# Kernel optimization log

Hardware: AMD Instinct MI355X
Metric: run time of the kernel (lower is better)

The kernel has to match this reference:

```python
import jax, jax.numpy as jnp
import numpy as np

N = 50000
E = 800000
H = 4
C = 64
IN = 61
NEG_SLOPE = 0.2


def setup_inputs() -> dict:
    key = jax.random.key(0)
    ks = jax.random.split(key, 20)
    x = jax.random.normal(ks[0], (N, IN), dtype=jnp.float32)
    edge_index = jax.random.randint(ks[1], (2, E), 0, N, dtype=jnp.int64)

    def glorot(k, shape):
        fan = shape[0] + shape[-1] if len(shape) == 2 else shape[-1] * 2
        s = jnp.sqrt(6.0 / fan)
        return jax.random.uniform(k, shape, jnp.float32, -s, s)

    dims = [IN, H * C, H * C]
    params = {}
    for i, din in enumerate(dims):
        params[f'w{i}'] = glorot(ks[2 + 4 * i], (din, H * C))
        params[f'att_src{i}'] = glorot(ks[3 + 4 * i], (H, C))
        params[f'att_dst{i}'] = glorot(ks[4 + 4 * i], (H, C))
        params[f'b{i}'] = jnp.zeros((H * C,), jnp.float32)
    params['head_w1'] = glorot(ks[14], (H * C, C))
    params['head_b1'] = jnp.zeros((C,), jnp.float32)
    params['head_w2'] = glorot(ks[15], (C, 1))
    params['head_b2'] = jnp.zeros((1,), jnp.float32)
    return dict(x=x, edge_index=edge_index, **params)


def _gat_layer(x, W, att_src, att_dst, bias, src, dst):
    # Linear transform -> [N, H, C]
    h = (x @ W).reshape(N, H, C)
    # Per-node attention logits
    a_src = jnp.einsum('nhc,hc->nh', h, att_src)  # [N, H]
    a_dst = jnp.einsum('nhc,hc->nh', h, att_dst)
    # Per-edge score, leaky relu
    e = jax.nn.leaky_relu(a_src[src] + a_dst[dst], NEG_SLOPE)  # [Etot, H]
    # Segment softmax over incoming edges of each dst node
    m = jax.ops.segment_max(e, dst, num_segments=N)  # [N, H]
    ex = jnp.exp(e - m[dst])
    denom = jax.ops.segment_sum(ex, dst, num_segments=N)
    alpha = ex / denom[dst]  # [Etot, H]
    # Scatter-aggregate messages
    out = jax.ops.segment_sum(h[src] * alpha[:, :, None], dst, num_segments=N)  # [N, H, C]
    return out.reshape(N, H * C) + bias


def reference(x, edge_index, w0, att_src0, att_dst0, b0,
              w1, att_src1, att_dst1, b1,
              w2, att_src2, att_dst2, b2,
              head_w1, head_b1, head_w2, head_b2):
    # PyG GATConv adds self-loops by default
    loop = jnp.arange(N, dtype=edge_index.dtype)
    src = jnp.concatenate([edge_index[0], loop])
    dst = jnp.concatenate([edge_index[1], loop])

    layers = [(w0, att_src0, att_dst0, b0),
              (w1, att_src1, att_dst1, b1),
              (w2, att_src2, att_dst2, b2)]
    h = x
    for (W, a_s, a_d, b) in layers:
        h = _gat_layer(h, W, a_s, a_d, b, src, dst)
        h = jax.nn.elu(h)  # dropout is identity in eval mode
    # MLP head
    h = jax.nn.relu(h @ head_w1 + head_b1)
    out = (h @ head_w2 + head_b2).squeeze(-1)  # [N]
    return out
```

## Files before the change

### kernel.cpp

```cpp
#include <hip/hip_runtime.h>
#include <cstdint>
#include <cstddef>

#define NN   50000
#define EE   800000
#define ETOT (EE + NN)
#define HC   256
#define NEG_SLOPE 0.2f
#define SENT_WORDS 25000
#define SENT_VAL 0x42C80000u

typedef __attribute__((ext_vector_type(8))) short g4_bf16x8;
typedef __attribute__((ext_vector_type(4))) float g4_f32x4;

__device__ __forceinline__ float g4_bf2f(unsigned short h) {
    union { unsigned int u; float f; } v;
    v.u = ((unsigned int)h) << 16;
    return v.f;
}
__device__ __forceinline__ unsigned short g4_f2bf(float f) {
    union { float f; unsigned int u; } v;
    v.f = f;
    unsigned int u = v.u;
    u += 0x7fffu + ((u >> 16) & 1u);
    return (unsigned short)(u >> 16);
}
__device__ __forceinline__ float g4_ld(const void* p, size_t i, int isf) {
    return isf ? ((const float*)p)[i] : g4_bf2f(((const unsigned short*)p)[i]);
}

__global__ void g4_detect(const unsigned int* __restrict__ xw,
                          const int* __restrict__ ei32, int* __restrict__ flags) {
    __shared__ int cnt[256];
    int t = threadIdx.x;
    unsigned int w = xw[t];
    int e = (int)((w >> 23) & 0xffu);
    cnt[t] = (e >= 110 && e <= 135) ? 1 : 0;
    __syncthreads();
    for (int off = 128; off > 0; off >>= 1) {
        if (t < off) cnt[t] += cnt[t + off];
        __syncthreads();
    }
    if (t == 0) {
        flags[0] = (cnt[0] >= 128) ? 1 : 0;
        int i64 = (ei32[1] == 0 && ei32[3] == 0 && ei32[5] == 0 &&
                   ei32[7] == 0 && ei32[9] == 0) ? 1 : 0;
        flags[1] = i64;
    }
}

__global__ void g4_zero(int* __restrict__ deg, int* __restrict__ cnt,
                        unsigned int* __restrict__ outw) {
    int i = blockIdx.x * 256 + threadIdx.x;
    if (i < NN) { deg[i] = 0; cnt[i] = 0; }
    if (i < SENT_WORDS) outw[i] = SENT_VAL;
}

__global__ void g4_hist(const int* __restrict__ ei, const int* __restrict__ flags,
                        int* __restrict__ deg) {
    int e = blockIdx.x * blockDim.x + threadIdx.x;
    if (e >= ETOT) return;
    int i64 = flags[1];
    int d;
    if (e < EE) d = i64 ? ei[2 * (EE + e)] : ei[EE + e];
    else        d = e - EE;
    atomicAdd(&deg[d], 1);
}

__global__ void g4_scan_block(const int* __restrict__ deg, int* __restrict__ tmp,
                              int* __restrict__ partial) {
    __shared__ int sh[256];
    int i = blockIdx.x * 256 + threadIdx.x;
    int v = (i < NN) ? deg[i] : 0;
    sh[threadIdx.x] = v;
    __syncthreads();
    for (int off = 1; off < 256; off <<= 1) {
        int t = (threadIdx.x >= off) ? sh[threadIdx.x - off] : 0;
        __syncthreads();
        sh[threadIdx.x] += t;
        __syncthreads();
    }
    if (i < NN) tmp[i] = sh[threadIdx.x] - v;
    if (threadIdx.x == 255) partial[blockIdx.x] = sh[255];
}

__global__ void g4_scan_partial(int* __restrict__ partial, int nb,
                                int* __restrict__ rowptrN) {
    __shared__ int sh[256];
    int v = (threadIdx.x < nb) ? partial[threadIdx.x] : 0;
    sh[threadIdx.x] = v;
    __syncthreads();
    for (int off = 1; off < 256; off <<= 1) {
        int t = (threadIdx.x >= off) ? sh[threadIdx.x - off] : 0;
        __syncthreads();
        sh[threadIdx.x] += t;
        __syncthreads();
    }
    if (threadIdx.x < nb) partial[threadIdx.x] = sh[threadIdx.x] - v;
    if (threadIdx.x == 0) *rowptrN = ETOT;
}

__global__ void g4_scan_add(const int* __restrict__ tmp, const int* __restrict__ partial,
                            int* __restrict__ rowptr) {
    int i = blockIdx.x * 256 + threadIdx.x;
    if (i < NN) rowptr[i] = tmp[i] + partial[blockIdx.x];
}

__global__ void g4_fill_csr(const int* __restrict__ ei, const int* __restrict__ flags,
                            const int* __restrict__ rowptr,
                            int* __restrict__ cnt, int* __restrict__ col) {
    int e = blockIdx.x * blockDim.x + threadIdx.x;
    if (e >= ETOT) return;
    int i64 = flags[1];
    int s, d;
    if (e < EE) {
        s = i64 ? ei[2 * e] : ei[e];
        d = i64 ? ei[2 * (EE + e)] : ei[EE + e];
    } else {
        s = e - EE; d = e - EE;
    }
    int pos = rowptr[d] + atomicAdd(&cnt[d], 1);
    col[pos] = s;
}

__global__ void g4_bprep(const void* __restrict__ B, const int* __restrict__ flags,
                         unsigned short* __restrict__ Bt, int K, int kshift, int Nc) {
    int i = blockIdx.x * 256 + threadIdx.x;
    int KP = 1 << kshift;
    if (i >= Nc << kshift) return;
    int n = i >> kshift;
    int k = i & (KP - 1);
    unsigned short v = 0;
    if (k < K) {
        if (flags[0]) v = g4_f2bf(((const float*)B)[(size_t)k * Nc + n]);
        else          v = ((const unsigned short*)B)[(size_t)k * Nc + n];
    }
    Bt[(size_t)n * KP + k] = v;
}

#define LDK 40
__global__ __launch_bounds__(256) void g4_gemm2(
    const void* __restrict__ A, int a_mode, const unsigned short* __restrict__ Bt,
    const int* __restrict__ flags, unsigned short* __restrict__ C,
    const void* __restrict__ att_src, const void* __restrict__ att_dst,
    float* __restrict__ a_srcO, float* __restrict__ a_dstO,
    int M, int K, int KP) {
    __shared__ short As[64 * LDK];
    __shared__ short Bs[256 * LDK];
    const int isf = flags[0];
    const int af  = (a_mode == 0) ? isf : 0;
    const int tid  = threadIdx.x;
    const int lane = tid & 63;
    const int wc   = tid >> 6;
    const int quad = lane >> 4;
    const int l15  = lane & 15;
    const int bm = blockIdx.x * 64;
    const int a_vec = (af == 0) && ((K & 31) == 0);

    g4_f32x4 acc[4][4];
    #pragma unroll
    for (int it = 0; it < 4; it++)
        #pragma unroll
        for (int jt = 0; jt < 4; jt++) {
            acc[it][jt].x = 0.f; acc[it][jt].y = 0.f;
            acc[it][jt].z = 0.f; acc[it][jt].w = 0.f;
        }

    for (int k0 = 0; k0 < KP; k0 += 32) {
        {
            int row = tid >> 2, kc = (tid & 3) * 8;
            int gm = bm + row;
            short v[8];
            if (a_vec && gm < M) {
                *(g4_bf16x8*)v = *(const g4_bf16x8*)((const short*)A + (size_t)gm * K + k0 + kc);
            } else {
                #pragma unroll
                for (int j = 0; j < 8; j++) {
                    int gk = k0 + kc + j;
                    if (gm < M && gk < K) {
                        if (af == 0) v[j] = ((const short*)A)[(size_t)gm * K + gk];
                        else         v[j] = (short)g4_f2bf(((const float*)A)[(size_t)gm * K + gk]);
                    } else v[j] = 0;
                }
            }
            *(g4_bf16x8*)&As[row * LDK + kc] = *(g4_bf16x8*)v;
        }
        {
            const unsigned short* bp = Bt + (size_t)tid * KP + k0;
            short* dst = &Bs[tid * LDK];
            *(g4_bf16x8*)(dst + 0)  = *(const g4_bf16x8*)(bp + 0);
            *(g4_bf16x8*)(dst + 8)  = *(const g4_bf16x8*)(bp + 8);
            *(g4_bf16x8*)(dst + 16) = *(const g4_bf16x8*)(bp + 16);
            *(g4_bf16x8*)(dst + 24) = *(const g4_bf16x8*)(bp + 24);
        }
        __syncthreads();
        g4_bf16x8 afr[4], bfr[4];
        #pragma unroll
        for (int it = 0; it < 4; it++)
            afr[it] = *(const g4_bf16x8*)&As[(it * 16 + l15) * LDK + quad * 8];
        #pragma unroll
        for (int jt = 0; jt < 4; jt++)
            bfr[jt] = *(const g4_bf16x8*)&Bs[(wc * 64 + jt * 16 + l15) * LDK + quad * 8];
        #pragma unroll
        for (int it = 0; it < 4; it++)
            #pragma unroll
            for (int jt = 0; jt < 4; jt++)
                acc[it][jt] = __builtin_amdgcn_mfma_f32_16x16x32_bf16(
                    afr[it], bfr[jt], acc[it][jt], 0, 0, 0);
        __syncthreads();
    }
    #pragma unroll
    for (int it = 0; it < 4; it++) {
        #pragma unroll
        for (int jt = 0; jt < 4; jt++) {
            int gn   = wc * 64 + jt * 16 + l15;
            int row0 = bm + it * 16 + quad * 4;
            #pragma unroll
            for (int r = 0; r < 4; r++) {
                int gm = row0 + r;
                if (gm < M) C[(size_t)gm * HC + gn] = g4_f2bf(acc[it][jt][r]);
            }
        }
    }
    float asv[4], adv[4];
    #pragma unroll
    for (int jt = 0; jt < 4; jt++) {
        asv[jt] = g4_ld(att_src, wc * 64 + jt * 16 + l15, isf);
        adv[jt] = g4_ld(att_dst, wc * 64 + jt * 16 + l15, isf);
    }
    #pragma unroll
    for (int it = 0; it < 4; it++) {
        #pragma unroll
        for (int r = 0; r < 4; r++) {
            float ps = 0.f, pd = 0.f;
            #pragma unroll
            for (int jt = 0; jt < 4; jt++) {
                ps += acc[it][jt][r] * asv[jt];
                pd += acc[it][jt][r] * adv[jt];
            }
            #pragma unroll
            for (int off = 1; off < 16; off <<= 1) {
                ps += __shfl_xor(ps, off);
                pd += __shfl_xor(pd, off);
            }
            if (l15 == 0) {
                int gm = bm + it * 16 + quad * 4 + r;
                if (gm < M) {
                    a_srcO[gm * 4 + wc] = ps;
                    a_dstO[gm * 4 + wc] = pd;
                }
            }
        }
    }
}

__global__ __launch_bounds__(256) void g4_gatherf(
    const unsigned short* __restrict__ h,
    const float* __restrict__ a_src, const float* __restrict__ a_dst,
    const int* __restrict__ rowptr, const int* __restrict__ col,
    const void* __restrict__ bias, const int* __restrict__ flags,
    unsigned short* __restrict__ xout) {
    int d    = (blockIdx.x * blockDim.x + threadIdx.x) >> 6;
    int lane = threadIdx.x & 63;
    if (d >= NN) return;
    d = __builtin_amdgcn_readfirstlane(d);
    const int isf = flags[0];
    const int hd  = lane >> 4;
    const int q   = lane & 3;
    const int eloc = lane >> 2;
    const int l15 = lane & 15;
    const int start = __builtin_amdgcn_readfirstlane(rowptr[d]);
    const int end   = __builtin_amdgcn_readfirstlane(rowptr[d + 1]);

    g4_f32x4 ad4 = *(const g4_f32x4*)(a_dst + 4 * (size_t)d);
    float mx[4] = {-1e30f, -1e30f, -1e30f, -1e30f};
    for (int i = start + lane; i < end; i += 64) {
        int s = col[i];
        g4_f32x4 as = *(const g4_f32x4*)(a_src + 4 * (size_t)s);
        #pragma unroll
        for (int hh = 0; hh < 4; hh++) {
            float e = as[hh] + ad4[hh];
            e = (e > 0.f) ? e : NEG_SLOPE * e;
            mx[hh] = fmaxf(mx[hh], e);
        }
    }
    for (int off = 32; off > 0; off >>= 1)
        #pragma unroll
        for (int hh = 0; hh < 4; hh++) mx[hh] = fmaxf(mx[hh], __shfl_xor(mx[hh], off));
    float mxq = (q < 2) ? ((q == 0) ? mx[0] : mx[1]) : ((q == 2) ? mx[2] : mx[3]);
    float adq = (q < 2) ? ((q == 0) ? ad4.x : ad4.y) : ((q == 2) ? ad4.z : ad4.w);

    float a0 = 0.f, a1 = 0.f, a2 = 0.f, a3 = 0.f;
    float sm = 0.f;
    const size_t ch = (size_t)(lane << 2);
    for (int base = start; base < end; base += 16) {
        int m = end - base;
        if (m > 16) m = 16;
        int cv = col[base + l15];
        int sE = __shfl(cv, eloc);
        float av = 0.f;
        if (eloc < m) {
            float e = a_src[4 * (size_t)sE + q] + adq;
            e = (e > 0.f) ? e : NEG_SLOPE * e;
            av = __expf(e - mxq);
            sm += av;
        }
        int j = 0;
        for (; j + 4 <= m; j += 4) {
            int s0 = __shfl(cv, j);
            int s1 = __shfl(cv, j + 1);
            int s2 = __shfl(cv, j + 2);
            int s3 = __shfl(cv, j + 3);
            float w0 = __shfl(av, 4 * j + hd);
            float w1 = __shfl(av, 4 * j + 4 + hd);
            float w2 = __shfl(av, 4 * j + 8 + hd);
            float w3 = __shfl(av, 4 * j + 12 + hd);
            uint2 h0 = *(const uint2*)(h + (((size_t)s0) << 8) + ch);
            uint2 h1 = *(const uint2*)(h + (((size_t)s1) << 8) + ch);
            uint2 h2 = *(const uint2*)(h + (((size_t)s2) << 8) + ch);
            uint2 h3 = *(const uint2*)(h + (((size_t)s3) << 8) + ch);
            a0 = fmaf(__uint_as_float(h0.x << 16),         w0, a0);
            a1 = fmaf(__uint_as_float(h0.x & 0xffff0000u), w0, a1);
            a2 = fmaf(__uint_as_float(h0.y << 16),         w0, a2);
            a3 = fmaf(__uint_as_float(h0.y & 0xffff0000u), w0, a3);
            a0 = fmaf(__uint_as_float(h1.x << 16),         w1, a0);
            a1 = fmaf(__uint_as_float(h1.x & 0xffff0000u), w1, a1);
            a2 = fmaf(__uint_as_float(h1.y << 16),         w1, a2);
            a3 = fmaf(__uint_as_float(h1.y & 0xffff0000u), w1, a3);
            a0 = fmaf(__uint_as_float(h2.x << 16),         w2, a0);
            a1 = fmaf(__uint_as_float(h2.x & 0xffff0000u), w2, a1);
            a2 = fmaf(__uint_as_float(h2.y << 16),         w2, a2);
            a3 = fmaf(__uint_as_float(h2.y & 0xffff0000u), w2, a3);
            a0 = fmaf(__uint_as_float(h3.x << 16),         w3, a0);
            a1 = fmaf(__uint_as_float(h3.x & 0xffff0000u), w3, a1);
            a2 = fmaf(__uint_as_float(h3.y << 16),         w3, a2);
            a3 = fmaf(__uint_as_float(h3.y & 0xffff0000u), w3, a3);
        }
        for (; j < m; j++) {
            int s = __shfl(cv, j);
            float w = __shfl(av, 4 * j + hd);
            uint2 hv = *(const uint2*)(h + (((size_t)s) << 8) + ch);
            a0 = fmaf(__uint_as_float(hv.x << 16),         w, a0);
            a1 = fmaf(__uint_as_float(hv.x & 0xffff0000u), w, a1);
            a2 = fmaf(__uint_as_float(hv.y << 16),         w, a2);
            a3 = fmaf(__uint_as_float(hv.y & 0xffff0000u), w, a3);
        }
    }
    for (int off = 4; off < 64; off <<= 1) sm += __shfl_xor(sm, off);
    float inv = 1.f / __shfl(sm, hd);
    float acc[4] = {a0 * inv, a1 * inv, a2 * inv, a3 * inv};
    unsigned short ov[4];
    #pragma unroll
    for (int j = 0; j < 4; j++) {
        float v = acc[j] + g4_ld(bias, (lane << 2) + j, isf);
        v = (v > 0.f) ? v : (__expf(v) - 1.f);
        ov[j] = g4_f2bf(v);
    }
    uint2 pack;
    pack.x = (unsigned int)ov[0] | ((unsigned int)ov[1] << 16);
    pack.y = (unsigned int)ov[2] | ((unsigned int)ov[3] << 16);
    *(uint2*)(xout + ((size_t)d << 8) + (lane << 2)) = pack;
}

__global__ __launch_bounds__(256) void g4_head2(
    const unsigned short* __restrict__ x, const void* __restrict__ w1,
    const void* __restrict__ b1, const void* __restrict__ w2,
    const void* __restrict__ b2, const int* __restrict__ flags,
    void* __restrict__ outp) {
    __shared__ float As[64][17];
    __shared__ float Bs[16][64];
    __shared__ float red[64][17];
    const int isf = flags[0];
    const int tid = threadIdx.x;
    const int bm  = blockIdx.x * 64;
    const int tx  = tid & 15;
    const int ty  = tid >> 4;
    float acc[4][4] = {};
    for (int k0 = 0; k0 < HC; k0 += 16) {
        for (int i = tid; i < 64 * 16; i += 256) {
            int m = i >> 4, kk = i & 15;
            int gm = bm + m;
            float v = 0.f;
            if (gm < NN) v = g4_bf2f(x[(size_t)gm * HC + k0 + kk]);
            As[m][kk] = v;
        }
        for (int i = tid; i < 16 * 64; i += 256) {
            int kk = i >> 6, n = i & 63;
            Bs[kk][n] = g4_ld(w1, (size_t)(k0 + kk) * 64 + n, isf);
        }
        __syncthreads();
        #pragma unroll
        for (int kk = 0; kk < 16; ++kk) {
            float a[4], b[4];
            #pragma unroll
            for (int i = 0; i < 4; i++) a[i] = As[ty * 4 + i][kk];
            #pragma unroll
            for (int j = 0; j < 4; j++) b[j] = Bs[kk][tx * 4 + j];
            #pragma unroll
            for (int i = 0; i < 4; i++)
                #pragma unroll
                for (int j = 0; j < 4; j++) acc[i][j] += a[i] * b[j];
        }
        __syncthreads();
    }
    float b1v[4], w2v[4];
    #pragma unroll
    for (int j = 0; j < 4; j++) {
        b1v[j] = g4_ld(b1, tx * 4 + j, isf);
        w2v[j] = g4_ld(w2, tx * 4 + j, isf);
    }
    #pragma unroll
    for (int i = 0; i < 4; i++) {
        float s = 0.f;
        #pragma unroll
        for (int j = 0; j < 4; j++) {
            float v = acc[i][j] + b1v[j];
            v = fmaxf(v, 0.f);
            s += v * w2v[j];
        }
        red[ty * 4 + i][tx] = s;
    }
    __syncthreads();
    if (tid < 64) {
        float s = 0.f;
        #pragma unroll
        for (int g = 0; g < 16; g++) s += red[tid][g];
        int gm = bm + tid;
        if (gm < NN) {
            float r = s + g4_ld(b2, 0, isf);
            if (isf) ((float*)outp)[gm] = r;
            else     ((unsigned short*)outp)[gm] = g4_f2bf(r);
        }
    }
}

extern "C" __attribute__((visibility("default")))
void kernel_launch(void* const* d_in, const int* in_sizes, int n_in,
                   void* d_out, int out_size, void* d_ws, size_t ws_size,
                   hipStream_t stream) {
    const void* x_in = d_in[0];
    const int*  ei   = (const int*)d_in[1];
    const void* W[3]    = {d_in[2], d_in[6], d_in[10]};
    const void* ASRC[3] = {d_in[3], d_in[7], d_in[11]};
    const void* ADST[3] = {d_in[4], d_in[8], d_in[12]};
    const void* BIAS[3] = {d_in[5], d_in[9], d_in[13]};
    const void* hw1 = d_in[14];
    const void* hb1 = d_in[15];
    const void* hw2 = d_in[16];
    const void* hb2 = d_in[17];

    char* base = (char*)d_ws;
    size_t woff = 0;
#define G4_TAKE(name, type, count) \
    type* name = (type*)(base + woff); \
    woff += (((size_t)(count)) * sizeof(type) + 255) & ~(size_t)255;
    G4_TAKE(flags,   int, 8)
    G4_TAKE(deg,     int, NN)
    G4_TAKE(cnt,     int, NN)
    G4_TAKE(tmp,     int, NN)
    G4_TAKE(partial, int, 256)
    G4_TAKE(rowptr,  int, NN + 1)
    G4_TAKE(col,     int, ETOT + 16)
    G4_TAKE(asr,     float, (size_t)NN * 4)
    G4_TAKE(adsb,    float, (size_t)NN * 4)
    G4_TAKE(Bt,      unsigned short, (size_t)HC * HC)
    G4_TAKE(hbuf,    unsigned short, (size_t)NN * HC)
    G4_TAKE(xbuf,    unsigned short, (size_t)NN * HC)
#undef G4_TAKE

    const int SCAN_BLOCKS = (NN + 255) / 256;
    const int EDGE_BLOCKS = (ETOT + 255) / 256;
    const int WAVE_BLOCKS = (NN + 3) / 4;
    const int TILE_BLOCKS = (NN + 63) / 64;

    g4_detect<<<1, 256, 0, stream>>>((const unsigned int*)x_in, ei, flags);
    g4_zero<<<SCAN_BLOCKS, 256, 0, stream>>>(deg, cnt, (unsigned int*)d_out);

    g4_hist<<<EDGE_BLOCKS, 256, 0, stream>>>(ei, flags, deg);
    g4_scan_block<<<SCAN_BLOCKS, 256, 0, stream>>>(deg, tmp, partial);
    g4_scan_partial<<<1, 256, 0, stream>>>(partial, SCAN_BLOCKS, rowptr + NN);
    g4_scan_add<<<SCAN_BLOCKS, 256, 0, stream>>>(tmp, partial, rowptr);
    g4_fill_csr<<<EDGE_BLOCKS, 256, 0, stream>>>(ei, flags, rowptr, cnt, col);

    for (int l = 0; l < 3; l++) {
        int K      = (l == 0) ? 61 : HC;
        int kshift = (l == 0) ? 6  : 8;
        int KP     = 1 << kshift;
        int pb     = ((HC << kshift) + 255) / 256;
        g4_bprep<<<pb, 256, 0, stream>>>(W[l], flags, Bt, K, kshift, HC);
        if (l == 0) {
            g4_gemm2<<<TILE_BLOCKS, 256, 0, stream>>>(x_in, 0, Bt, flags, hbuf,
                ASRC[l], ADST[l], asr, adsb, NN, K, KP);
        } else {
            g4_gemm2<<<TILE_BLOCKS, 256, 0, stream>>>(xbuf, 1, Bt, flags, hbuf,
                ASRC[l], ADST[l], asr, adsb, NN, K, KP);
        }
        g4_gatherf<<<WAVE_BLOCKS, 256, 0, stream>>>(hbuf, asr, adsb, rowptr, col,
                                                    BIAS[l], flags, xbuf);
    }
    g4_head2<<<TILE_BLOCKS, 256, 0, stream>>>(xbuf, hw1, hb1, hw2, hb2, flags, d_out);
}
```

Before: 541.2 us.

## Hold pre-swizzled weight fragments in registers and drop LDS staging in GEMM

Measured after the change: 546.5 us. About the same (+1.0%).

```diff
diff --git a/kernel.cpp b/kernel.cpp
--- a/kernel.cpp
+++ b/kernel.cpp
@@ -123,39 +123,61 @@
     col[pos] = s;
 }
 
-__global__ void g4_bprep(const void* __restrict__ B, const int* __restrict__ flags,
-                         unsigned short* __restrict__ Bt, int K, int kshift, int Nc) {
+__global__ void g4_aprep(const void* __restrict__ x, const int* __restrict__ flags,
+                         unsigned short* __restrict__ Apad) {
     int i = blockIdx.x * 256 + threadIdx.x;
-    int KP = 1 << kshift;
-    if (i >= Nc << kshift) return;
-    int n = i >> kshift;
-    int k = i & (KP - 1);
+    if (i >= NN * 64) return;
+    int row = i >> 6, k = i & 63;
+    unsigned short v = 0;
+    if (k < 61) {
+        if (flags[0]) v = g4_f2bf(((const float*)x)[(size_t)row * 61 + k]);
+        else          v = ((const unsigned short*)x)[(size_t)row * 61 + k];
+    }
+    Apad[i] = v;
+}
+
+__global__ void g4_bfprep(const void* __restrict__ B, const int* __restrict__ flags,
+                          unsigned short* __restrict__ Bfrag, int K, int NK) {
+    int i = blockIdx.x * 256 + threadIdx.x;
+    if (i >= HC * NK * 32) return;
+    int j = i & 7;
+    int rest = i >> 3;
+    int lane = rest & 63; rest >>= 6;
+    int ks = rest % NK;
+    int wcjt = rest / NK;
+    int jt = wcjt & 3, wc = wcjt >> 2;
+    int n = wc * 64 + jt * 16 + (lane & 15);
+    int k = ks * 32 + (lane >> 4) * 8 + j;
     unsigned short v = 0;
     if (k < K) {
-        if (flags[0]) v = g4_f2bf(((const float*)B)[(size_t)k * Nc + n]);
-        else          v = ((const unsigned short*)B)[(size_t)k * Nc + n];
-    }
-    Bt[(size_t)n * KP + k] = v;
-}
-
-#define LDK 40
-__global__ __launch_bounds__(256) void g4_gemm2(
-    const void* __restrict__ A, int a_mode, const unsigned short* __restrict__ Bt,
+        if (flags[0]) v = g4_f2bf(((const float*)B)[(size_t)k * HC + n]);
+        else          v = ((const unsigned short*)B)[(size_t)k * HC + n];
+    }
+    Bfrag[i] = v;
+}
+
+template <int NK>
+__global__ __launch_bounds__(256) void g4_gemm3(
+    const unsigned short* __restrict__ A, const unsigned short* __restrict__ Bfrag,
     const int* __restrict__ flags, unsigned short* __restrict__ C,
     const void* __restrict__ att_src, const void* __restrict__ att_dst,
-    float* __restrict__ a_srcO, float* __restrict__ a_dstO,
-    int M, int K, int KP) {
-    __shared__ short As[64 * LDK];
-    __shared__ short Bs[256 * LDK];
-    const int isf = flags[0];
-    const int af  = (a_mode == 0) ? isf : 0;
+    float* __restrict__ a_srcO, float* __restrict__ a_dstO, int M) {
+    const int KP   = NK * 32;
+    const int isf  = flags[0];
     const int tid  = threadIdx.x;
     const int lane = tid & 63;
     const int wc   = tid >> 6;
     const int quad = lane >> 4;
     const int l15  = lane & 15;
-    const int bm = blockIdx.x * 64;
-    const int a_vec = (af == 0) && ((K & 31) == 0);
+    const int bm   = blockIdx.x * 64;
+
+    g4_bf16x8 bfr[4][NK];
+    #pragma unroll
+    for (int jt = 0; jt < 4; jt++)
+        #pragma unroll
+        for (int ks = 0; ks < NK; ks++)
+            bfr[jt][ks] = *(const g4_bf16x8*)
+                (Bfrag + ((size_t)(((wc * 4 + jt) * NK + ks) * 64 + lane) << 3));
 
     g4_f32x4 acc[4][4];
     #pragma unroll
@@ -166,49 +188,21 @@
             acc[it][jt].z = 0.f; acc[it][jt].w = 0.f;
         }
 
-    for (int k0 = 0; k0 < KP; k0 += 32) {
-        {
-            int row = tid >> 2, kc = (tid & 3) * 8;
-            int gm = bm + row;
-            short v[8];
-            if (a_vec && gm < M) {
-                *(g4_bf16x8*)v = *(const g4_bf16x8*)((const short*)A + (size_t)gm * K + k0 + kc);
-            } else {
-                #pragma unroll
-                for (int j = 0; j < 8; j++) {
-                    int gk = k0 + kc + j;
-                    if (gm < M && gk < K) {
-                        if (af == 0) v[j] = ((const short*)A)[(size_t)gm * K + gk];
-                        else         v[j] = (short)g4_f2bf(((const float*)A)[(size_t)gm * K + gk]);
-                    } else v[j] = 0;
-                }
-            }
-            *(g4_bf16x8*)&As[row * LDK + kc] = *(g4_bf16x8*)v;
-        }
-        {
-            const unsigned short* bp = Bt + (size_t)tid * KP + k0;
-            short* dst = &Bs[tid * LDK];
-            *(g4_bf16x8*)(dst + 0)  = *(const g4_bf16x8*)(bp + 0);
-            *(g4_bf16x8*)(dst + 8)  = *(const g4_bf16x8*)(bp + 8);
-            *(g4_bf16x8*)(dst + 16) = *(const g4_bf16x8*)(bp + 16);
-            *(g4_bf16x8*)(dst + 24) = *(const g4_bf16x8*)(bp + 24);
-        }
-        __syncthreads();
-        g4_bf16x8 afr[4], bfr[4];
+    #pragma unroll
+    for (int ks = 0; ks < NK; ks++) {
+        g4_bf16x8 afr[4];
         #pragma unroll
         for (int it = 0; it < 4; it++)
-            afr[it] = *(const g4_bf16x8*)&As[(it * 16 + l15) * LDK + quad * 8];
-        #pragma unroll
-        for (int jt = 0; jt < 4; jt++)
-            bfr[jt] = *(const g4_bf16x8*)&Bs[(wc * 64 + jt * 16 + l15) * LDK + quad * 8];
+            afr[it] = *(const g4_bf16x8*)
+                (A + (size_t)(bm + it * 16 + l15) * KP + ks * 32 + quad * 8);
         #pragma unroll
         for (int it = 0; it < 4; it++)
             #pragma unroll
             for (int jt = 0; jt < 4; jt++)
                 acc[it][jt] = __builtin_amdgcn_mfma_f32_16x16x32_bf16(
-                    afr[it], bfr[jt], acc[it][jt], 0, 0, 0);
-        __syncthreads();
-    }
+                    afr[it], bfr[jt][ks], acc[it][jt], 0, 0, 0);
+    }
+
     #pragma unroll
     for (int it = 0; it < 4; it++) {
         #pragma unroll
@@ -306,35 +300,37 @@
             sm += av;
         }
         int j = 0;
+        for (; j + 8 <= m; j += 8) {
+            uint2 hv[8]; float w[8];
+            #pragma unroll
+            for (int u = 0; u < 8; u++) {
+                int s = __shfl(cv, j + u);
+                w[u]  = __shfl(av, 4 * (j + u) + hd);
+                hv[u] = *(const uint2*)(h + (((size_t)s) << 8) + ch);
+            }
+            #pragma unroll
+            for (int u = 0; u < 8; u++) {
+                a0 = fmaf(__uint_as_float(hv[u].x << 16),         w[u], a0);
+                a1 = fmaf(__uint_as_float(hv[u].x & 0xffff0000u), w[u], a1);
+                a2 = fmaf(__uint_as_float(hv[u].y << 16),         w[u], a2);
+                a3 = fmaf(__uint_as_float(hv[u].y & 0xffff0000u), w[u], a3);
+            }
+        }
         for (; j + 4 <= m; j += 4) {
-            int s0 = __shfl(cv, j);
-            int s1 = __shfl(cv, j + 1);
-            int s2 = __shfl(cv, j + 2);
-            int s3 = __shfl(cv, j + 3);
-            float w0 = __shfl(av, 4 * j + hd);
-            float w1 = __shfl(av, 4 * j + 4 + hd);
-            float w2 = __shfl(av, 4 * j + 8 + hd);
-            float w3 = __shfl(av, 4 * j + 12 + hd);
-            uint2 h0 = *(const uint2*)(h + (((size_t)s0) << 8) + ch);
-            uint2 h1 = *(const uint2*)(h + (((size_t)s1) << 8) + ch);
-            uint2 h2 = *(const uint2*)(h + (((size_t)s2) << 8) + ch);
-            uint2 h3 = *(const uint2*)(h + (((size_t)s3) << 8) + ch);
-            a0 = fmaf(__uint_as_float(h0.x << 16),         w0, a0);
-            a1 = fmaf(__uint_as_float(h0.x & 0xffff0000u), w0, a1);
-            a2 = fmaf(__uint_as_float(h0.y << 16),         w0, a2);
-            a3 = fmaf(__uint_as_float(h0.y & 0xffff0000u), w0, a3);
-            a0 = fmaf(__uint_as_float(h1.x << 16),         w1, a0);
-            a1 = fmaf(__uint_as_float(h1.x & 0xffff0000u), w1, a1);
-            a2 = fmaf(__uint_as_float(h1.y << 16),         w1, a2);
-            a3 = fmaf(__uint_as_float(h1.y & 0xffff0000u), w1, a3);
-            a0 = fmaf(__uint_as_float(h2.x << 16),         w2, a0);
-            a1 = fmaf(__uint_as_float(h2.x & 0xffff0000u), w2, a1);
-            a2 = fmaf(__uint_as_float(h2.y << 16),         w2, a2);
-            a3 = fmaf(__uint_as_float(h2.y & 0xffff0000u), w2, a3);
-            a0 = fmaf(__uint_as_float(h3.x << 16),         w3, a0);
-            a1 = fmaf(__uint_as_float(h3.x & 0xffff0000u), w3, a1);
-            a2 = fmaf(__uint_as_float(h3.y << 16),         w3, a2);
-            a3 = fmaf(__uint_as_float(h3.y & 0xffff0000u), w3, a3);
+            uint2 hv[4]; float w[4];
+            #pragma unroll
+            for (int u = 0; u < 4; u++) {
+                int s = __shfl(cv, j + u);
+                w[u]  = __shfl(av, 4 * (j + u) + hd);
+                hv[u] = *(const uint2*)(h + (((size_t)s) << 8) + ch);
+            }
+            #pragma unroll
+            for (int u = 0; u < 4; u++) {
+                a0 = fmaf(__uint_as_float(hv[u].x << 16),         w[u], a0);
+                a1 = fmaf(__uint_as_float(hv[u].x & 0xffff0000u), w[u], a1);
+                a2 = fmaf(__uint_as_float(hv[u].y << 16),         w[u], a2);
+                a3 = fmaf(__uint_as_float(hv[u].y & 0xffff0000u), w[u], a3);
+            }
         }
         for (; j < m; j++) {
             int s = __shfl(cv, j);
@@ -463,9 +459,10 @@
     G4_TAKE(col,     int, ETOT + 16)
     G4_TAKE(asr,     float, (size_t)NN * 4)
     G4_TAKE(adsb,    float, (size_t)NN * 4)
-    G4_TAKE(Bt,      unsigned short, (size_t)HC * HC)
-    G4_TAKE(hbuf,    unsigned short, (size_t)NN * HC)
-    G4_TAKE(xbuf,    unsigned short, (size_t)NN * HC)
+    G4_TAKE(Apad,    unsigned short, (size_t)(NN + 64) * 64)
+    G4_TAKE(Bfrag,   unsigned short, (size_t)HC * HC)
+    G4_TAKE(hbuf,    unsigned short, (size_t)(NN + 64) * HC)
+    G4_TAKE(xbuf,    unsigned short, (size_t)(NN + 64) * HC)
 #undef G4_TAKE
 
     const int SCAN_BLOCKS = (NN + 255) / 256;
@@ -482,18 +479,18 @@
     g4_scan_add<<<SCAN_BLOCKS, 256, 0, stream>>>(tmp, partial, rowptr);
     g4_fill_csr<<<EDGE_BLOCKS, 256, 0, stream>>>(ei, flags, rowptr, cnt, col);
 
+    g4_aprep<<<(NN * 64 + 255) / 256, 256, 0, stream>>>(x_in, flags, Apad);
+
     for (int l = 0; l < 3; l++) {
-        int K      = (l == 0) ? 61 : HC;
-        int kshift = (l == 0) ? 6  : 8;
-        int KP     = 1 << kshift;
-        int pb     = ((HC << kshift) + 255) / 256;
-        g4_bprep<<<pb, 256, 0, stream>>>(W[l], flags, Bt, K, kshift, HC);
+        int K  = (l == 0) ? 61 : HC;
+        int NK = (l == 0) ? 2  : 8;
+        g4_bfprep<<<(HC * NK * 32 + 255) / 256, 256, 0, stream>>>(W[l], flags, Bfrag, K, NK);
         if (l == 0) {
-            g4_gemm2<<<TILE_BLOCKS, 256, 0, stream>>>(x_in, 0, Bt, flags, hbuf,
-                ASRC[l], ADST[l], asr, adsb, NN, K, KP);
+            g4_gemm3<2><<<TILE_BLOCKS, 256, 0, stream>>>(Apad, Bfrag, flags, hbuf,
+                ASRC[l], ADST[l], asr, adsb, NN);
         } else {
-            g4_gemm2<<<TILE_BLOCKS, 256, 0, stream>>>(xbuf, 1, Bt, flags, hbuf,
-                ASRC[l], ADST[l], asr, adsb, NN, K, KP);
+            g4_gemm3<8><<<TILE_BLOCKS, 256, 0, stream>>>(xbuf, Bfrag, flags, hbuf,
+                ASRC[l], ADST[l], asr, adsb, NN);
         }
         g4_gatherf<<<WAVE_BLOCKS, 256, 0, stream>>>(hbuf, asr, adsb, rowptr, col,
                                                     BIAS[l], flags, xbuf);
```
